# Optimization experiments

Hardware: AMD Instinct MI355X
Metric: run time of the kernel (lower is better)

The kernel has to match this reference:

```python
import jax, jax.numpy as jnp
import numpy as np
import math

D = 128  # embedding_dim, hard-coded in source


def setup_inputs() -> dict:
    key = jax.random.key(0)
    k1, k2, k3, k4, k5 = jax.random.split(key, 5)
    B, S = 4, 4096
    x = jax.random.normal(k1, (B, S, D), dtype=jnp.float32)
    token_attention_masks = jax.random.randint(k2, (B, S), 0, 2).astype(jnp.int64)
    # torch.rand -> uniform [0,1)
    w_query = jax.random.uniform(k3, (D, D), dtype=jnp.float32)
    w_key = jax.random.uniform(k4, (D, D), dtype=jnp.float32)
    w_value = jax.random.uniform(k5, (D, D), dtype=jnp.float32)
    return {
        "x": x,
        "token_attention_masks": token_attention_masks,
        "w_query": w_query,
        "w_key": w_key,
        "w_value": w_value,
    }


def reference(x, token_attention_masks, w_query, w_key, w_value):
    # QKV projections (single head, no bias)
    query = jnp.einsum('bsd,de->bse', x, w_query)
    key = jnp.einsum('bsd,de,->bse', x, w_key, jnp.float32(1.0)) if False else jnp.einsum('bsd,de->bse', x, w_key)
    value = jnp.einsum('bsd,de->bse', x, w_value)
    dk = key.shape[2]
    scale = jnp.einsum('bqd,bkd->bqk', query, key) / math.sqrt(dk)  # [B,S,S]
    # NOTE: the original module computes an additive mask (`new_scale`) but
    # applies softmax to the UNMASKED `scale` (a bug in the source); we
    # replicate the actual output math faithfully, so the mask is unused.
    attention_probability = jax.nn.softmax(scale, axis=2)
    attention_output = jnp.einsum('bqk,bkd->bqd', attention_probability, value)
    return attention_output
```

## Files before the change

### kernel.cpp

```cpp
#include <hip/hip_runtime.h>
#include <math.h>

#define BATCH  4
#define SEQ    4096
#define DIM    128
#define NROW   (BATCH*SEQ)
#define NSPLIT 8
#define NW     384

typedef _Float16 f16_t;
typedef _Float16 f16x2  __attribute__((ext_vector_type(2)));
typedef _Float16 f16x4  __attribute__((ext_vector_type(4)));
typedef _Float16 f16x8  __attribute__((ext_vector_type(8)));
typedef _Float16 f16x16 __attribute__((ext_vector_type(16)));
typedef float    f32x4  __attribute__((ext_vector_type(4)));
typedef float    f32x16 __attribute__((ext_vector_type(16)));

#define QSCALE ((float)(1.4426950408889634 / 11.313708498984761))

__global__ __launch_bounds__(256) void wsplit_kernel(
    const float* __restrict__ wq, const float* __restrict__ wk,
    const float* __restrict__ wv,
    f16_t* __restrict__ Wth, f16_t* __restrict__ Wtl)
{
    const int idx = blockIdx.x*256 + threadIdx.x;
    const int n = idx >> 7;
    const int k = idx & 127;
    const int mat = n >> 7, col = n & 127;
    const float* w = (mat == 0) ? wq : ((mat == 1) ? wk : wv);
    const float v = w[k*DIM + col];
    const f16_t h = (f16_t)v;
    Wth[idx] = h;
    Wtl[idx] = (f16_t)(v - (float)h);
}

#define LDX 72
#define LDE 136

__global__ __launch_bounds__(256) void proj_kernel(
    const float* __restrict__ x,
    const f16_t* __restrict__ Wth, const f16_t* __restrict__ Wtl,
    f16_t* __restrict__ Qh, f16_t* __restrict__ Kh, f16_t* __restrict__ Vt)
{
    __shared__ __align__(16) f16_t smem[(64 + 64 + 128 + 128) * LDX];
    f16_t* sXh = smem;
    f16_t* sXl = smem + 64*LDX;
    f16_t* sWh = smem + 128*LDX;
    f16_t* sWl = smem + 256*LDX;

    const int tid  = threadIdx.x;
    const int wave = tid >> 6;
    const int lane = tid & 63;
    const int quad = lane >> 4;
    const int ln   = lane & 15;

    const int nt = blockIdx.x % 3;
    const int mb = blockIdx.x / 3;
    const int m0 = mb * 64;
    const int n0 = nt * 128;

    f32x4 acc[8];
    #pragma unroll
    for (int nb = 0; nb < 8; nb++)
        for (int r = 0; r < 4; r++) acc[nb][r] = 0.f;

    #pragma unroll
    for (int ph = 0; ph < 2; ph++) {
        __syncthreads();
        #pragma unroll
        for (int i = 0; i < 4; i++) {
            const int idx = tid + 256*i;
            const int r = idx >> 4, f4 = idx & 15;
            const float4 v = *(const float4*)(x + (size_t)(m0+r)*DIM + ph*64 + f4*4);
            f16_t h0=(f16_t)v.x, h1=(f16_t)v.y, h2=(f16_t)v.z, h3=(f16_t)v.w;
            *(f16x4*)(sXh + r*LDX + f4*4) = (f16x4){h0,h1,h2,h3};
            *(f16x4*)(sXl + r*LDX + f4*4) =
                (f16x4){(f16_t)(v.x-(float)h0),(f16_t)(v.y-(float)h1),
                        (f16_t)(v.z-(float)h2),(f16_t)(v.w-(float)h3)};
        }
        #pragma unroll
        for (int i = 0; i < 4; i++) {
            const int idx = tid + 256*i;
            const int n = idx >> 3, g = idx & 7;
            *(uint4*)(sWh + n*LDX + g*8) =
                *(const uint4*)(Wth + (size_t)(n0+n)*DIM + ph*64 + g*8);
            *(uint4*)(sWl + n*LDX + g*8) =
                *(const uint4*)(Wtl + (size_t)(n0+n)*DIM + ph*64 + g*8);
        }
        __syncthreads();

        f16x8 ah[2], al[2];
        #pragma unroll
        for (int ks = 0; ks < 2; ks++) {
            ah[ks] = *(const f16x8*)(sXh + (wave*16+ln)*LDX + quad*8 + ks*32);
            al[ks] = *(const f16x8*)(sXl + (wave*16+ln)*LDX + quad*8 + ks*32);
        }
        #pragma unroll
        for (int nb = 0; nb < 8; nb++) {
            #pragma unroll
            for (int ks = 0; ks < 2; ks++) {
                const f16x8 bh = *(const f16x8*)(sWh + (nb*16+ln)*LDX + quad*8 + ks*32);
                const f16x8 bl = *(const f16x8*)(sWl + (nb*16+ln)*LDX + quad*8 + ks*32);
                acc[nb] = __builtin_amdgcn_mfma_f32_16x16x32_f16(ah[ks], bh, acc[nb], 0,0,0);
                acc[nb] = __builtin_amdgcn_mfma_f32_16x16x32_f16(al[ks], bh, acc[nb], 0,0,0);
                acc[nb] = __builtin_amdgcn_mfma_f32_16x16x32_f16(ah[ks], bl, acc[nb], 0,0,0);
            }
        }
    }

    __syncthreads();

    if (nt != 2) {
        const float scale = (nt == 0) ? QSCALE : 1.0f;
        f16_t* dsth = (nt == 0) ? Qh : Kh;
        f16_t* sH = smem;
        #pragma unroll
        for (int nb = 0; nb < 8; nb++)
            #pragma unroll
            for (int r = 0; r < 4; r++) {
                const int row  = wave*16 + quad*4 + r;
                const int colp = (nb*16 + ln) ^ (quad << 4);
                sH[row*LDE + colp] = (f16_t)(acc[nb][r] * scale);
            }
        __syncthreads();
        #pragma unroll
        for (int jj = 0; jj < 4; jj++) {
            const int c    = tid + 256*jj;
            const int row  = c >> 4;
            const int col  = (c & 15) * 8;
            const int colp = col ^ (((row >> 2) & 3) << 4);
            *(uint4*)(dsth + (size_t)(m0 + row)*DIM + col) =
                *(const uint4*)(sH + row*LDE + colp);
        }
    } else {
        f16_t* svt = smem;
        const int rowl = wave*16 + quad*4;
        #pragma unroll
        for (int nb = 0; nb < 8; nb++)
            for (int r = 0; r < 4; r++)
                svt[(nb*16+ln)*LDX + rowl + r] = (f16_t)acc[nb][r];
        __syncthreads();
        const int bb = m0 >> 12, sloc = m0 & (SEQ-1);
        const int d = tid >> 1, half = tid & 1;
        #pragma unroll
        for (int q = 0; q < 4; q++) {
            *(uint4*)(Vt + ((size_t)bb*DIM + d)*SEQ + sloc + half*32 + q*8) =
                *(const uint4*)(svt + d*LDX + half*32 + q*8);
        }
    }
}

#define LDK 136
#define LDV 68
#define LDO 132

__global__ __launch_bounds__(256, 3) void flash_kernel(
    const f16_t* __restrict__ Qh, const f16_t* __restrict__ Kh,
    const f16_t* __restrict__ Vt,
    f16_t* __restrict__ Opart, float2* __restrict__ mlbuf)
{
    __shared__ __align__(16) f16_t smem[64*LDK + 128*LDV];
    f16_t* sK = smem;
    f16_t* sV = smem + 64*LDK;

    const int tid  = threadIdx.x;
    const int wave = tid >> 6;
    const int lane = tid & 63;
    const int l31  = lane & 31;
    const int h    = lane >> 5;

    const int grp = blockIdx.x & 31;
    const int b   = grp >> 3;
    const int sp  = grp & 7;
    const int qt  = blockIdx.x >> 5;
    const int q0  = qt*128 + wave*32;

    f16x8 qf[8];
    {
        const f16_t* gq = Qh + ((size_t)b*SEQ + q0 + l31)*DIM + h*8;
        #pragma unroll
        for (int ks = 0; ks < 8; ks++)
            qf[ks] = *(const f16x8*)(gq + ks*16);
    }

    f32x16 oacc[4];
    #pragma unroll
    for (int mb = 0; mb < 4; mb++)
        #pragma unroll
        for (int r = 0; r < 16; r++) oacc[mb][r] = 0.f;
    float mrun = -__builtin_inff(), lrun = 0.f;

    const int kr = tid >> 4;
    const int kc = (tid & 15) * 8;
    const int vd = tid >> 3;
    const int vj = (tid & 7) * 8;

    const f16_t* gK = Kh + (size_t)b*SEQ*DIM;
    const f16_t* gV = Vt + (size_t)b*DIM*SEQ;

    for (int kt = sp*8; kt < sp*8 + 8; kt++) {
        float4 pk[4], pv[4];
        {
            const f16_t* gk = gK + (size_t)kt*64*DIM;
            const f16_t* gv = gV + kt*64;
            #pragma unroll
            for (int p = 0; p < 4; p++)
                pk[p] = *(const float4*)(gk + (kr + 16*p)*DIM + kc);
            #pragma unroll
            for (int p = 0; p < 4; p++)
                pv[p] = *(const float4*)(gv + (size_t)(vd + 32*p)*SEQ + vj);
        }
        __syncthreads();
        #pragma unroll
        for (int p = 0; p < 4; p++)
            *(uint4*)(sK + (kr+16*p)*LDK + kc) = __builtin_bit_cast(uint4, pk[p]);
        #pragma unroll
        for (int p = 0; p < 4; p++) {
            const f16x8 w = __builtin_bit_cast(f16x8, pv[p]);
            *(f16x4*)(sV + (vd+32*p)*LDV + vj    ) = __builtin_shufflevector(w, w, 0,1,2,3);
            *(f16x4*)(sV + (vd+32*p)*LDV + vj + 4) = __builtin_shufflevector(w, w, 4,5,6,7);
        }
        __syncthreads();

        f32x16 sacc[2];
        #pragma unroll
        for (int sb = 0; sb < 2; sb++)
            #pragma unroll
            for (int r = 0; r < 16; r++) sacc[sb][r] = 0.f;
        #pragma unroll
        for (int ks = 0; ks < 8; ks++) {
            #pragma unroll
            for (int sb = 0; sb < 2; sb++) {
                const f16x8 af = *(const f16x8*)(sK + (sb*32 + l31)*LDK + ks*16 + h*8);
                sacc[sb] = __builtin_amdgcn_mfma_f32_32x32x16_f16(af, qf[ks], sacc[sb], 0,0,0);
            }
        }

        float mx = sacc[0][0];
        #pragma unroll
        for (int sb = 0; sb < 2; sb++)
            #pragma unroll
            for (int r = 0; r < 16; r++) mx = fmaxf(mx, sacc[sb][r]);
        mx = fmaxf(mx, __shfl_xor(mx, 32, 64));
        const float mnew = fmaxf(mrun, mx);

        if (__any(mnew > mrun)) {
            const float alpha = __builtin_amdgcn_exp2f(mrun - mnew);
            lrun *= alpha;
            #pragma unroll
            for (int mb = 0; mb < 4; mb++)
                #pragma unroll
                for (int r = 0; r < 16; r++) oacc[mb][r] *= alpha;
            mrun = mnew;
        }

        union PBuf { f16x2 p2[8]; f16x8 v8[2]; } pbf[2];
        float rs = 0.f;
        #pragma unroll
        for (int sb = 0; sb < 2; sb++)
            #pragma unroll
            for (int r2 = 0; r2 < 8; r2++) {
                const float e0 = __builtin_amdgcn_exp2f(sacc[sb][2*r2]   - mnew);
                const float e1 = __builtin_amdgcn_exp2f(sacc[sb][2*r2+1] - mnew);
                rs += e0 + e1;
                pbf[sb].p2[r2] = __builtin_bit_cast(f16x2,
                    __builtin_amdgcn_cvt_pkrtz(e0, e1));
            }
        rs += __shfl_xor(rs, 32, 64);
        lrun += rs;

        #pragma unroll
        for (int t = 0; t < 4; t++) {
            const f16x8 pb = pbf[t>>1].v8[t&1];
            #pragma unroll
            for (int mb = 0; mb < 4; mb++) {
                const f16_t* va = sV + (mb*32 + l31)*LDV + t*16 + h*4;
                const f16x4 a0 = *(const f16x4*)(va);
                const f16x4 a1 = *(const f16x4*)(va + 8);
                const f16x8 af = __builtin_shufflevector(a0, a1, 0,1,2,3,4,5,6,7);
                oacc[mb] = __builtin_amdgcn_mfma_f32_32x32x16_f16(af, pb, oacc[mb], 0,0,0);
            }
        }
    }

    __syncthreads();
    const float invl = 1.f / lrun;
    f16_t* sOw = smem + wave*32*LDO;
    #pragma unroll
    for (int mb = 0; mb < 4; mb++)
        #pragma unroll
        for (int rp = 0; rp < 8; rp++) {
            const int r0 = rp*2;
            const int d  = mb*32 + (r0 & 3) + 8*(r0 >> 2) + 4*h;
            union { f16_t f[2]; unsigned u; } pkv;
            pkv.f[0] = (f16_t)(oacc[mb][r0]   * invl);
            pkv.f[1] = (f16_t)(oacc[mb][r0+1] * invl);
            *(unsigned*)(sOw + l31*LDO + d) = pkv.u;
        }
    __asm__ volatile("s_waitcnt lgkmcnt(0)" ::: "memory");

    const size_t gb = ((size_t)sp*NROW + (size_t)b*SEQ + q0)*DIM;
    #pragma unroll
    for (int jj = 0; jj < 8; jj++) {
        const int c  = lane + 64*jj;
        const int q  = c >> 4;
        const int dc = (c & 15)*8;
        union { f16x4 v[2]; uint4 u; } o;
        o.v[0] = *(const f16x4*)(sOw + q*LDO + dc);
        o.v[1] = *(const f16x4*)(sOw + q*LDO + dc + 4);
        *(uint4*)(Opart + gb + (size_t)q*DIM + dc) = o.u;
    }
    if (h == 0)
        mlbuf[sp*NROW + b*SEQ + q0 + l31] = make_float2(mrun, lrun);
}

__global__ __launch_bounds__(256) void combine_kernel(
    const f16_t* __restrict__ Opart, const float2* __restrict__ mlbuf,
    float* __restrict__ out)
{
    const int idx = blockIdx.x*256 + threadIdx.x;
    const int row = idx >> 4;
    const int d0  = (idx & 15) * 8;

    float m[NSPLIT], l[NSPLIT];
    #pragma unroll
    for (int s = 0; s < NSPLIT; s++) {
        const float2 v = mlbuf[s*NROW + row];
        m[s] = v.x; l[s] = v.y;
    }
    float M = m[0];
    #pragma unroll
    for (int s = 1; s < NSPLIT; s++) M = fmaxf(M, m[s]);
    float w[NSPLIT], denom = 0.f;
    #pragma unroll
    for (int s = 0; s < NSPLIT; s++) {
        w[s] = l[s] * __builtin_amdgcn_exp2f(m[s] - M);
        denom += w[s];
    }
    const float inv = 1.f / denom;

    float o[8] = {0,0,0,0,0,0,0,0};
    #pragma unroll
    for (int s = 0; s < NSPLIT; s++) {
        const f16x8 v = *(const f16x8*)(Opart + ((size_t)s*NROW + row)*DIM + d0);
        const float ws = w[s] * inv;
        #pragma unroll
        for (int j = 0; j < 8; j++) o[j] += ws * (float)v[j];
    }
    float* ob = out + (size_t)row*DIM + d0;
    *(float4*)(ob)     = make_float4(o[0], o[1], o[2], o[3]);
    *(float4*)(ob + 4) = make_float4(o[4], o[5], o[6], o[7]);
}

extern "C" void kernel_launch(void* const* d_in, const int* in_sizes, int n_in,
                              void* d_out, int out_size, void* d_ws, size_t ws_size,
                              hipStream_t stream) {
    const float* x  = (const float*)d_in[0];
    const float* wq = (const float*)d_in[2];
    const float* wk = (const float*)d_in[3];
    const float* wv = (const float*)d_in[4];

    f16_t* ws = (f16_t*)d_ws;
    f16_t* Qh    = ws;
    f16_t* Kh    = Qh  + (size_t)NROW*DIM;
    f16_t* Vt    = Kh  + (size_t)NROW*DIM;
    f16_t* Wth   = Vt  + (size_t)NROW*DIM;
    f16_t* Wtl   = Wth + (size_t)NW*DIM;
    f16_t* Opart = Wtl + (size_t)NW*DIM;
    float2* mlbuf = (float2*)(Opart + (size_t)NSPLIT*NROW*DIM);

    wsplit_kernel <<<NW*DIM/256,            256, 0, stream>>>(wq, wk, wv, Wth, Wtl);
    proj_kernel   <<<(NROW/64)*3,           256, 0, stream>>>(x, Wth, Wtl, Qh, Kh, Vt);
    flash_kernel  <<<BATCH*(SEQ/128)*NSPLIT,256, 0, stream>>>(Qh, Kh, Vt, Opart, mlbuf);
    combine_kernel<<<NROW*DIM/8/256,        256, 0, stream>>>(Opart, mlbuf, (float*)d_out);
}
```

Before: 125.3 us.

## Fuse split-KV combine into flash kernel via atomic counter and halve split count

The number of key splits drops from 8 to 4, so each flash block walks 16 key tiles instead of 8 and writes half as many partial outputs. The separate combine kernel is removed. The last block to finish a query tile, found with an atomic counter reset by a memset, merges the partial results directly. This removes one kernel launch and cuts partial-buffer traffic, but the grid shrinks from 1024 to 512 blocks, which may leave CUs underused, and the merging block now does serialized tail work.

```diff
diff --git a/kernel.cpp b/kernel.cpp
--- a/kernel.cpp
+++ b/kernel.cpp
@@ -5,7 +5,7 @@
 #define SEQ    4096
 #define DIM    128
 #define NROW   (BATCH*SEQ)
-#define NSPLIT 8
+#define NSPLIT 4
 #define NW     384
 
 typedef _Float16 f16_t;
@@ -157,11 +157,13 @@
 __global__ __launch_bounds__(256, 3) void flash_kernel(
     const f16_t* __restrict__ Qh, const f16_t* __restrict__ Kh,
     const f16_t* __restrict__ Vt,
-    f16_t* __restrict__ Opart, float2* __restrict__ mlbuf)
+    f16_t* __restrict__ Opart, float2* __restrict__ mlbuf,
+    int* __restrict__ cnt, float* __restrict__ out)
 {
     __shared__ __align__(16) f16_t smem[64*LDK + 128*LDV];
     f16_t* sK = smem;
     f16_t* sV = smem + 64*LDK;
+    __shared__ int sMerge;
 
     const int tid  = threadIdx.x;
     const int wave = tid >> 6;
@@ -169,10 +171,10 @@
     const int l31  = lane & 31;
     const int h    = lane >> 5;
 
-    const int grp = blockIdx.x & 31;
-    const int b   = grp >> 3;
-    const int sp  = grp & 7;
-    const int qt  = blockIdx.x >> 5;
+    const int grp = blockIdx.x & 15;
+    const int b   = grp >> 2;
+    const int sp  = grp & 3;
+    const int qt  = blockIdx.x >> 4;
     const int q0  = qt*128 + wave*32;
 
     f16x8 qf[8];
@@ -198,7 +200,7 @@
     const f16_t* gK = Kh + (size_t)b*SEQ*DIM;
     const f16_t* gV = Vt + (size_t)b*DIM*SEQ;
 
-    for (int kt = sp*8; kt < sp*8 + 8; kt++) {
+    for (int kt = sp*16; kt < sp*16 + 16; kt++) {
         float4 pk[4], pv[4];
         {
             const f16_t* gk = gK + (size_t)kt*64*DIM;
@@ -312,44 +314,49 @@
     }
     if (h == 0)
         mlbuf[sp*NROW + b*SEQ + q0 + l31] = make_float2(mrun, lrun);
-}
-
-__global__ __launch_bounds__(256) void combine_kernel(
-    const f16_t* __restrict__ Opart, const float2* __restrict__ mlbuf,
-    float* __restrict__ out)
-{
-    const int idx = blockIdx.x*256 + threadIdx.x;
-    const int row = idx >> 4;
-    const int d0  = (idx & 15) * 8;
-
-    float m[NSPLIT], l[NSPLIT];
-    #pragma unroll
-    for (int s = 0; s < NSPLIT; s++) {
-        const float2 v = mlbuf[s*NROW + row];
-        m[s] = v.x; l[s] = v.y;
-    }
-    float M = m[0];
-    #pragma unroll
-    for (int s = 1; s < NSPLIT; s++) M = fmaxf(M, m[s]);
-    float w[NSPLIT], denom = 0.f;
-    #pragma unroll
-    for (int s = 0; s < NSPLIT; s++) {
-        w[s] = l[s] * __builtin_amdgcn_exp2f(m[s] - M);
-        denom += w[s];
-    }
-    const float inv = 1.f / denom;
-
-    float o[8] = {0,0,0,0,0,0,0,0};
-    #pragma unroll
-    for (int s = 0; s < NSPLIT; s++) {
-        const f16x8 v = *(const f16x8*)(Opart + ((size_t)s*NROW + row)*DIM + d0);
-        const float ws = w[s] * inv;
-        #pragma unroll
-        for (int j = 0; j < 8; j++) o[j] += ws * (float)v[j];
-    }
-    float* ob = out + (size_t)row*DIM + d0;
-    *(float4*)(ob)     = make_float4(o[0], o[1], o[2], o[3]);
-    *(float4*)(ob + 4) = make_float4(o[4], o[5], o[6], o[7]);
+
+    __threadfence();
+    __syncthreads();
+    if (tid == 0)
+        sMerge = (atomicAdd(&cnt[b*32 + qt], 1) == NSPLIT - 1);
+    __syncthreads();
+    if (sMerge) {
+        __threadfence();
+        const int brow = b*SEQ + qt*128;
+        #pragma unroll
+        for (int i = 0; i < 8; i++) {
+            const int u   = tid + 256*i;
+            const int row = brow + (u >> 4);
+            const int d0  = (u & 15) * 8;
+            float m[NSPLIT], l[NSPLIT];
+            #pragma unroll
+            for (int s = 0; s < NSPLIT; s++) {
+                const float2 v = mlbuf[s*NROW + row];
+                m[s] = v.x; l[s] = v.y;
+            }
+            float M = m[0];
+            #pragma unroll
+            for (int s = 1; s < NSPLIT; s++) M = fmaxf(M, m[s]);
+            float w[NSPLIT], denom = 0.f;
+            #pragma unroll
+            for (int s = 0; s < NSPLIT; s++) {
+                w[s] = l[s] * __builtin_amdgcn_exp2f(m[s] - M);
+                denom += w[s];
+            }
+            const float inv = 1.f / denom;
+            float o[8] = {0,0,0,0,0,0,0,0};
+            #pragma unroll
+            for (int s = 0; s < NSPLIT; s++) {
+                const f16x8 v = *(const f16x8*)(Opart + ((size_t)s*NROW + row)*DIM + d0);
+                const float ws = w[s] * inv;
+                #pragma unroll
+                for (int j = 0; j < 8; j++) o[j] += ws * (float)v[j];
+            }
+            float* ob = out + (size_t)row*DIM + d0;
+            *(float4*)(ob)     = make_float4(o[0], o[1], o[2], o[3]);
+            *(float4*)(ob + 4) = make_float4(o[4], o[5], o[6], o[7]);
+        }
+    }
 }
 
 extern "C" void kernel_launch(void* const* d_in, const int* in_sizes, int n_in,
@@ -368,9 +375,11 @@
     f16_t* Wtl   = Wth + (size_t)NW*DIM;
     f16_t* Opart = Wtl + (size_t)NW*DIM;
     float2* mlbuf = (float2*)(Opart + (size_t)NSPLIT*NROW*DIM);
-
+    int*    cnt   = (int*)(mlbuf + (size_t)NSPLIT*NROW);
+
+    hipMemsetAsync(cnt, 0, 128*sizeof(int), stream);
     wsplit_kernel <<<NW*DIM/256,            256, 0, stream>>>(wq, wk, wv, Wth, Wtl);
     proj_kernel   <<<(NROW/64)*3,           256, 0, stream>>>(x, Wth, Wtl, Qh, Kh, Vt);
-    flash_kernel  <<<BATCH*(SEQ/128)*NSPLIT,256, 0, stream>>>(Qh, Kh, Vt, Opart, mlbuf);
-    combine_kernel<<<NROW*DIM/8/256,        256, 0, stream>>>(Opart, mlbuf, (float*)d_out);
+    flash_kernel  <<<BATCH*(SEQ/128)*NSPLIT,256, 0, stream>>>(Qh, Kh, Vt, Opart, mlbuf,
+                                                              cnt, (float*)d_out);
 }
```

New measurement: 223.4 us. +78.3%, slower.
